# Kernel optimization log

Measured on AMD Instinct MI355X. Metric: run time of the kernel, lower is better.

Reference implementation:

```python
import jax, jax.numpy as jnp
import numpy as np

NS, NV, NB, L = 64, 32, 8, 4      # scalar channels, vector channels, bessel bases, layers
EMB = 32                           # atom-type embedding dim
MAX_R = 3.0                        # cutoff radius
NUM_NEIGH = 32.0                   # avg degree used for scatter normalization
N, E = 10000, 320000
NW = NS * 2 + NV * 2               # per-edge tensor-product weights from radial MLP
MAX_TYPES = 10


def smooth_cutoff(x):
    # e3nn md-example smooth_cutoff: 1 for x<0.5, 0 for x>1, cosine blend between
    u = 2.0 * (x - 1.0)
    y = (1.0 - jnp.cos(jnp.pi * u)) * 0.5
    y = jnp.where(u > 0.0, 0.0, y)
    y = jnp.where(u < -1.0, 1.0, y)
    return y


def bessel_basis(r):
    # soft_one_hot_linspace(basis='bessel', cutoff=False) * sqrt(NB)
    n = jnp.arange(1, NB + 1, dtype=r.dtype)
    y = jnp.sqrt(2.0 / MAX_R) * jnp.sin(n * jnp.pi * r[:, None] / MAX_R) / r[:, None]
    return y * np.sqrt(NB).astype(np.float32)


def edge_info(x, src, dst):
    feats, attrs = [], []
    for i in range(2):  # nvec = x.shape[-1] // 3 = 2
        vec = x[src, 3 * i:3 * i + 3] - x[dst, 3 * i:3 * i + 3]  # [E,3]
        r = jnp.linalg.norm(vec, axis=1)
        sh = np.float32(np.sqrt(3.0)) * vec / r[:, None]          # 1x1o SH, component norm
        feats.append(bessel_basis(r))
        attrs.append(smooth_cutoff(r / MAX_R)[:, None] * sh)
    return jnp.concatenate(feats, axis=-1), jnp.stack(attrs, axis=1)  # [E,2*NB], [E,2,3]


def _forward(x, emb_table, W_up, W_proj, fc1, b1, fc2, W_sv, W_vs, W_sc_s, W_sc_v, Ws, Wv, h, mix, node_attr, edge_src, edge_dst):
    n = x.shape[0]
    inv_nb = np.float32(1.0 / np.sqrt(NUM_NEIGH))
    # uplift: 2 input vectors -> NV hidden vectors, NS hidden scalars (zero init)
    xv = x.reshape(n, 2, 3)
    v = jnp.einsum('nic,iv->nvc', xv, W_up)        # [n,NV,3]
    s = jnp.zeros((n, NS), x.dtype)                # [n,NS]
    s_old, v_old = s, v
    attr_emb = emb_table[node_attr]                # [n,EMB]
    xcur = x
    for i in range(L):
        f, a = edge_info(xcur, edge_src, edge_dst)            # [E,2NB], [E,2,3]
        w = jax.nn.silu(f @ fc1[i] + b1[i]) @ fc2[i]          # [E,NW] radial TP weights
        w1 = w[:, :NS * 2].reshape(-1, NS, 2)                 # 0e x 1o -> 1o path weights
        w2 = w[:, NS * 2:].reshape(-1, NV, 2)                 # 1o x 1o -> 0e path weights
        # equivariant tensor-product messages (gather at edge_src)
        t = s[edge_src][:, :, None] * w1                      # [E,NS,2]
        q = jnp.einsum('euv,uvm->evm', t, W_sv[i])            # [E,2,NV]
        msg_v = jnp.einsum('evm,evc->emc', q, a)              # [E,NV,3]
        d = jnp.einsum('euc,evc->euv', v[edge_src], a)        # [E,NV,2]
        msg_s = jnp.einsum('euv,uvm->em', d * w2, W_vs[i])    # [E,NS+NV]
        # scatter-add at edge_dst, normalized by sqrt(num_neighbors)
        agg_s = jnp.zeros((n, NS + NV), x.dtype).at[edge_dst].add(msg_s) * inv_nb
        agg_v = jnp.zeros((n, NV, 3), x.dtype).at[edge_dst].add(msg_v) * inv_nb
        # self-connection: fully-connected TP with node-attr scalars
        sc_s = jnp.einsum('nu,ne,uem->nm', s, attr_emb, W_sc_s[i])
        sc_v = jnp.einsum('nuc,ne,uev->nvc', v, attr_emb, W_sc_v[i])
        cs = sc_s + agg_s
        cv = sc_v + agg_v
        # Gate: silu on scalars, sigmoid gate scalars modulate vectors
        gs = jax.nn.silu(cs[:, :NS])
        gate = jax.nn.sigmoid(cs[:, NS:])
        gv = cv * gate[:, :, None]
        # self-interaction (equivariant linear per degree)
        si_s = s @ Ws[i]
        si_v = jnp.einsum('nuc,uv->nvc', v, Wv[i])
        # verlet-like update
        hi2 = h[i] ** 2
        s_new = 2.0 * s - s_old + hi2 * (mix[i] * gs + (mix[i] - 1.0) * si_s)
        v_new = 2.0 * v - v_old + hi2 * (mix[i] * gv + (mix[i] - 1.0) * si_v)
        s_old, v_old = s, v
        s, v = s_new, v_new
        # project back to x for next layer's edge features
        xcur = jnp.einsum('nvc,vi->nic', v, W_proj).reshape(n, 6)
    return xcur


def setup_inputs() -> dict:
    key = jax.random.key(0)
    ks = jax.random.split(key, 20)
    x = jax.random.normal(ks[0], (N, 6), jnp.float32)
    node_attr = jax.random.randint(ks[1], (N,), 0, MAX_TYPES)
    edge_src = jax.random.randint(ks[2], (E,), 0, N)
    off = jax.random.randint(ks[3], (E,), 1, N)
    edge_dst = (edge_src + off) % N  # no self-loops -> no zero edge_vec
    batch = jnp.zeros((N,), jnp.int32)
    rn = lambda k, sh, sc: jax.random.normal(k, sh, jnp.float32) * np.float32(sc)
    emb_table = rn(ks[4], (MAX_TYPES, EMB), 0.5)
    W_up = rn(ks[5], (2, NV), 1.0 / np.sqrt(2))
    W_proj = rn(ks[6], (NV, 2), 1.0 / np.sqrt(NV))
    fc1 = rn(ks[7], (L, 2 * NB, 64), 1.0 / np.sqrt(2 * NB))
    b1 = jnp.zeros((L, 64), jnp.float32)
    fc2 = rn(ks[8], (L, 64, NW), 1.0 / np.sqrt(64))
    W_sv = rn(ks[9], (L, NS, 2, NV), 1.0 / np.sqrt(NS * 2))
    W_vs = rn(ks[10], (L, NV, 2, NS + NV), 1.0 / np.sqrt(NV * 2))
    W_sc_s = rn(ks[11], (L, NS, EMB, NS + NV), 1.0 / np.sqrt(NS * EMB))
    W_sc_v = rn(ks[12], (L, NV, EMB, NV), 1.0 / np.sqrt(NV * EMB))
    Ws = rn(ks[13], (L, NS, NS), 1.0 / np.sqrt(NS))
    Wv = rn(ks[14], (L, NV, NV), 1.0 / np.sqrt(NV))
    h = jnp.ones((L,), jnp.float32) * 0.01
    mix = jnp.ones((L,), jnp.float32) * 0.5
    return {"x": x, "emb_table": emb_table, "W_up": W_up, "W_proj": W_proj, "fc1": fc1, "b1": b1, "fc2": fc2, "W_sv": W_sv, "W_vs": W_vs, "W_sc_s": W_sc_s, "W_sc_v": W_sc_v, "Ws": Ws, "Wv": Wv, "h": h, "mix": mix, "node_attr": node_attr, "edge_src": edge_src, "edge_dst": edge_dst, "batch": batch}


def reference(x, emb_table, W_up, W_proj, fc1, b1, fc2, W_sv, W_vs, W_sc_s, W_sc_v, Ws, Wv, h, mix, node_attr, edge_src, edge_dst, batch):
    return _forward(x, emb_table, W_up, W_proj, fc1, b1, fc2, W_sv, W_vs, W_sc_s, W_sc_v, Ws, Wv, h, mix, node_attr, edge_src, edge_dst)
```

## Files before the change

### kernel.cpp

```cpp
#include <hip/hip_runtime.h>
#include <math.h>

constexpr int cNS = 64, cNV = 32, cNB = 8, cL = 4, cEMB = 32, cNT = 10;
constexpr float PI_F = 3.14159265358979323846f;
constexpr float INV_SQRT_NN = 0.17677669529663687f;
constexpr float BESSEL_C = 2.3094010767585034f;
constexpr float SQRT3 = 1.7320508075688772f;

typedef unsigned short u16;
typedef unsigned int u32;
typedef unsigned long long u64;
typedef __attribute__((ext_vector_type(8))) short bf16x8;
typedef __attribute__((ext_vector_type(4))) float f32x4;
typedef __attribute__((ext_vector_type(2))) float f32x2;
typedef __attribute__((ext_vector_type(4))) int i32x4;

__device__ __forceinline__ u16 f2b(float x) {
  u32 u = __float_as_uint(x);
  return (u16)((u + 0x7fffu + ((u >> 16) & 1u)) >> 16);
}
__device__ __forceinline__ float b2f(u16 h) { return __uint_as_float(((u32)h) << 16); }
__device__ __forceinline__ float blo(u32 w) { return __uint_as_float(w << 16); }
__device__ __forceinline__ float bhi(u32 w) { return __uint_as_float(w & 0xffff0000u); }

__device__ __forceinline__ u32 pkbf(float lo, float hi) {
  u32 r;
  asm("v_cvt_pk_bf16_f32 %0, %1, %2" : "=v"(r) : "v"(lo), "v"(hi));
  return r;
}

__device__ __forceinline__ void lds_fence() {
  asm volatile("s_waitcnt lgkmcnt(0)" ::: "memory");
  __builtin_amdgcn_sched_barrier(0);
}

union U8 { bf16x8 v; u32 w[4]; };

__device__ __forceinline__ f32x4 mfma16(bf16x8 a, bf16x8 b, f32x4 c) {
  return __builtin_amdgcn_mfma_f32_16x16x32_bf16(a, b, c, 0, 0, 0);
}


__global__ void k_precompA(const float* __restrict__ emb, const float* __restrict__ Wss,
                           float* __restrict__ A) {
  int idx = blockIdx.x * 256 + threadIdx.x;
  if (idx >= cL * cNT * 64 * 96) return;
  int m = idx % 96;
  int u = (idx / 96) % 64;
  int t = (idx / (96 * 64)) % cNT;
  int l = idx / (96 * 64 * cNT);
  float acc = 0.f;
#pragma unroll
  for (int e = 0; e < 32; ++e)
    acc += emb[t * 32 + e] * Wss[((size_t)(l * 64 + u) * 32 + e) * 96 + m];
  A[idx] = acc;
}

__global__ void k_precompB(const float* __restrict__ emb, const float* __restrict__ Wsv_,
                           float* __restrict__ B) {
  int idx = blockIdx.x * 256 + threadIdx.x;
  if (idx >= cL * cNT * 32 * 32) return;
  int vo = idx % 32;
  int u = (idx / 32) % 32;
  int t = (idx / 1024) % cNT;
  int l = idx / (1024 * cNT);
  float acc = 0.f;
#pragma unroll
  for (int e = 0; e < 32; ++e)
    acc += emb[t * 32 + e] * Wsv_[((size_t)(l * 32 + u) * 32 + e) * 32 + vo];
  B[idx] = acc;
}

__global__ void k_packB(const float* __restrict__ fc2, const float* __restrict__ Wsv,
                        const float* __restrict__ Wvs, const float* __restrict__ fc1,
                        u16* __restrict__ fc2L, u16* __restrict__ WsvL,
                        u16* __restrict__ WvsL, u16* __restrict__ fc1L) {
  int idx = blockIdx.x * 256 + threadIdx.x;
  const int T1 = cL * 12288, T2 = cL * 2 * 2048, T3 = cL * 2 * 3072, T4 = cL * 2048;
  if (idx < T1) {
    int l = idx / 12288, r = idx % 12288;
    int ki = r & 7, tt = r >> 3;
    int nn = tt % 192, kq = tt / 192;
    fc2L[idx] = f2b(fc2[((size_t)(l * 64) + kq * 8 + ki) * 192 + nn]);
  } else if (idx < T1 + T2) {
    int r0 = idx - T1;
    int l = r0 / 4096, r1 = r0 % 4096;
    int k2 = r1 / 2048, r = r1 % 2048;
    int ki = r & 7, tt = r >> 3;
    int mm = tt % 32, kq = tt / 32;
    WsvL[r0] = f2b(Wsv[((size_t)((l * 64 + kq * 8 + ki) * 2) + k2) * 32 + mm]);
  } else if (idx < T1 + T2 + T3) {
    int r0 = idx - T1 - T2;
    int l = r0 / 6144, r1 = r0 % 6144;
    int k2 = r1 / 3072, r = r1 % 3072;
    int ki = r & 7, tt = r >> 3;
    int mm = tt % 96, kq = tt / 96;
    WvsL[r0] = f2b(Wvs[((size_t)((l * 32 + kq * 8 + ki) * 2) + k2) * 96 + mm]);
  } else if (idx < T1 + T2 + T3 + T4) {
    int r0 = idx - T1 - T2 - T3;
    int l = r0 / 2048, r1 = r0 % 2048;
    int kq = r1 / 512, rem = r1 % 512;
    int n = rem / 8, ki = rem & 7;
    fc1L[r0] = (kq < 2) ? f2b(fc1[l * 1024 + (kq * 8 + ki) * 64 + n]) : (u16)0;
  }
}

__global__ void k_init(const float* __restrict__ x, const float* __restrict__ Wup,
                       float* __restrict__ v, float* __restrict__ v_old,
                       float* __restrict__ xcur, int N) {
  int idx = blockIdx.x * 256 + threadIdx.x;
  if (idx >= N * 32) return;
  int n = idx >> 5, vc = idx & 31;
  float w0 = Wup[vc], w1 = Wup[32 + vc];
#pragma unroll
  for (int c = 0; c < 3; ++c) {
    float val = x[n * 6 + c] * w0 + x[n * 6 + 3 + c] * w1;
    v[idx * 3 + c] = val;
    v_old[idx * 3 + c] = val;
  }
  if (vc < 6) xcur[n * 6 + vc] = x[n * 6 + vc];
}


__global__ void k_zero_i(int* __restrict__ p, int n) {
  int i = blockIdx.x * 256 + threadIdx.x;
  if (i < n) p[i] = 0;
}

__global__ void k_hist(const int* __restrict__ edst, int* __restrict__ deg, int E) {
  int e = blockIdx.x * 256 + threadIdx.x;
  if (e < E) atomicAdd(&deg[edst[e]], 1);
}

__global__ __launch_bounds__(1024) void k_scan(const int* __restrict__ deg,
                                               int* __restrict__ row_ptr,
                                               int* __restrict__ cursor, int N) {
  __shared__ int part[1024];
  int t = threadIdx.x;
  int chunk = (N + 1023) / 1024;
  int base = t * chunk;
  int sum = 0;
  for (int i = 0; i < chunk; ++i) {
    int idx = base + i;
    if (idx < N) sum += deg[idx];
  }
  part[t] = sum;
  __syncthreads();
  for (int off = 1; off < 1024; off <<= 1) {
    int val = (t >= off) ? part[t - off] : 0;
    __syncthreads();
    part[t] += val;
    __syncthreads();
  }
  int run = (t > 0) ? part[t - 1] : 0;
  for (int i = 0; i < chunk; ++i) {
    int idx = base + i;
    if (idx < N) {
      row_ptr[idx] = run;
      cursor[idx] = run;
      run += deg[idx];
    }
  }
  if (t == 1023) row_ptr[N] = part[1023];
}

__global__ void k_scatter(const int* __restrict__ esrc, const int* __restrict__ edst,
                          int* __restrict__ cursor, int* __restrict__ esrc_s,
                          int* __restrict__ edst_s, int E) {
  int e = blockIdx.x * 256 + threadIdx.x;
  if (e < E) {
    int d = edst[e];
    int p = atomicAdd(&cursor[d], 1);
    esrc_s[p] = esrc[e];
    edst_s[p] = d;
  }
}

template <bool SZERO>
__global__ __launch_bounds__(128) void k_edge_mfma(
    const float* __restrict__ xcur, const float* __restrict__ s, const float* __restrict__ v,
    const int* __restrict__ esrc_s, const int* __restrict__ edst_s,
    const u16* __restrict__ fc1L, const float* __restrict__ b1,
    const u16* __restrict__ fc2L, const u16* __restrict__ WsvL0,
    const u16* __restrict__ WsvL1, const u16* __restrict__ WvsL0,
    const u16* __restrict__ WvsL1, u16* __restrict__ msgbuf, int E) {
  __shared__ u16 wbAll[2][32 * 200];
  __shared__ float aAll[2][32][6];
  int wid = threadIdx.x >> 6, lane = threadIdx.x & 63;
  int e0 = (blockIdx.x * 2 + wid) * 32;
  if (e0 >= E) return;
  u16* wb = wbAll[wid];
  int lrow = lane & 15, lg = lane >> 4;

  {
    int el = lane >> 1, qq = lane & 1;
    int ge = e0 + el;
    if (ge >= E) ge = E - 1;
    int gs = esrc_s[ge], gd = edst_s[ge];
    const float* ps = xcur + (size_t)gs * 6 + qq * 3;
    const float* pd = xcur + (size_t)gd * 6 + qq * 3;
    float vx = ps[0] - pd[0];
    float vy = ps[1] - pd[1];
    float vz = ps[2] - pd[2];
    float r2 = vx * vx + vy * vy + vz * vz;
    float rr = sqrtf(r2);
    float invr = 1.0f / rr;
    float th = (PI_F / 3.0f) * rr;
    float s1, c1;
    __sincosf(th, &s1, &c1);
    float twc = 2.0f * c1;
    float snm = 0.f, sn = s1;
    float fc = BESSEL_C * invr;
    float f8[8];
#pragma unroll
    for (int nn = 0; nn < 8; ++nn) {
      f8[nn] = fc * sn;
      float nx = twc * sn - snm;
      snm = sn;
      sn = nx;
    }
    float uu = (2.0f / 3.0f) * rr - 2.0f;
    float cut;
    if (uu > 0.f) cut = 0.f;
    else if (uu < -1.f) cut = 1.f;
    else cut = (1.0f - __cosf(PI_F * uu)) * 0.5f;
    float sc = cut * SQRT3 * invr;
    u32* fp = (u32*)(wb + 5120 + el * 40);
#pragma unroll
    for (int i = 0; i < 4; ++i) fp[qq * 4 + i] = pkbf(f8[2 * i], f8[2 * i + 1]);
#pragma unroll
    for (int i = 0; i < 4; ++i) fp[8 + qq * 4 + i] = 0u;
    float* ap = aAll[wid][el];
    ap[qq * 3 + 0] = vx * sc;
    ap[qq * 3 + 1] = vy * sc;
    ap[qq * 3 + 2] = vz * sc;
  }
  lds_fence();

  {
    bf16x8 fA0 = *(const bf16x8*)(wb + 5120 + lrow * 40 + lg * 8);
    bf16x8 fA1 = *(const bf16x8*)(wb + 5120 + (16 + lrow) * 40 + lg * 8);
    f32x4 hp0[4], hp1[4];
#pragma unroll
    for (int nb = 0; nb < 4; ++nb) {
      bf16x8 bB = *(const bf16x8*)(fc1L + (size_t)(lg * 64 + nb * 16 + lrow) * 8);
      f32x4 z = {0.f, 0.f, 0.f, 0.f};
      hp0[nb] = mfma16(fA0, bB, z);
      hp1[nb] = mfma16(fA1, bB, z);
    }
#pragma unroll
    for (int nb = 0; nb < 4; ++nb) {
      float bias = b1[nb * 16 + lrow];
      int col = nb * 16 + lrow;
      {
        float hv[4];
#pragma unroll
        for (int r = 0; r < 4; ++r) {
          float xv = hp0[nb][r] + bias;
          hv[r] = xv * (1.0f / (1.0f + __expf(-xv)));
        }
        u32 p01 = pkbf(hv[0], hv[1]);
        u32 p23 = pkbf(hv[2], hv[3]);
        wb[(4 * lg + 0) * 72 + col] = (u16)p01;
        wb[(4 * lg + 1) * 72 + col] = (u16)(p01 >> 16);
        wb[(4 * lg + 2) * 72 + col] = (u16)p23;
        wb[(4 * lg + 3) * 72 + col] = (u16)(p23 >> 16);
      }
      {
        float hv[4];
#pragma unroll
        for (int r = 0; r < 4; ++r) {
          float xv = hp1[nb][r] + bias;
          hv[r] = xv * (1.0f / (1.0f + __expf(-xv)));
        }
        u32 p01 = pkbf(hv[0], hv[1]);
        u32 p23 = pkbf(hv[2], hv[3]);
        wb[(16 + 4 * lg + 0) * 72 + col] = (u16)p01;
        wb[(16 + 4 * lg + 1) * 72 + col] = (u16)(p01 >> 16);
        wb[(16 + 4 * lg + 2) * 72 + col] = (u16)p23;
        wb[(16 + 4 * lg + 3) * 72 + col] = (u16)(p23 >> 16);
      }
    }
  }
  lds_fence();

  bf16x8 ha0 = *(const bf16x8*)(wb + lrow * 72 + lg * 8);
  bf16x8 hbf0 = *(const bf16x8*)(wb + lrow * 72 + 32 + lg * 8);
  bf16x8 ha1 = *(const bf16x8*)(wb + (16 + lrow) * 72 + lg * 8);
  bf16x8 hbf1 = *(const bf16x8*)(wb + (16 + lrow) * 72 + 32 + lg * 8);
  lds_fence();

  int xw = lg << 3;
#pragma unroll
  for (int nb = (SZERO ? 8 : 0); nb < 12; ++nb) {
    bf16x8 b0 = *(const bf16x8*)(fc2L + (size_t)(lg * 192 + nb * 16 + lrow) * 8);
    bf16x8 b1v = *(const bf16x8*)(fc2L + (size_t)((4 + lg) * 192 + nb * 16 + lrow) * 8);
    f32x4 z = {0.f, 0.f, 0.f, 0.f};
    f32x4 c0 = mfma16(ha0, b0, z);
    c0 = mfma16(hbf0, b1v, c0);
    f32x4 c1 = mfma16(ha1, b0, z);
    c1 = mfma16(hbf1, b1v, c1);
    int n = nb * 16 + lrow;
    int pn = (n < 128) ? ((n & 1) * 64 + (n >> 1)) : (128 + (n & 1) * 32 + ((n - 128) >> 1));
    int cx = pn ^ xw;
    {
      int rb = (4 * lg) * 200 + cx;
      u32 p01 = pkbf(c0[0], c0[1]);
      u32 p23 = pkbf(c0[2], c0[3]);
      wb[rb] = (u16)p01;
      wb[rb + 200] = (u16)(p01 >> 16);
      wb[rb + 400] = (u16)p23;
      wb[rb + 600] = (u16)(p23 >> 16);
    }
    {
      int rb = (16 + 4 * lg) * 200 + cx;
      u32 p01 = pkbf(c1[0], c1[1]);
      u32 p23 = pkbf(c1[2], c1[3]);
      wb[rb] = (u16)p01;
      wb[rb + 200] = (u16)(p01 >> 16);
      wb[rb + 400] = (u16)p23;
      wb[rb + 600] = (u16)(p23 >> 16);
    }
  }
  lds_fence();

  const u16* wrow0 = wb + lrow * 200 + (((lg ^ (lrow >> 2)) & 3) << 3);
  const u16* wrow1 = wrow0 + 3200;

  int prow0 = e0 + lrow;
  if (prow0 >= E) prow0 = E - 1;
  int prow1 = e0 + 16 + lrow;
  if (prow1 >= E) prow1 = E - 1;
  int srcs[2] = {esrc_s[prow0], esrc_s[prow1]};

  f32x4 q0[2][2], q1[2][2];
  if (!SZERO) {
    U8 t0a[2], t0b[2], t1a[2], t1b[2];
#pragma unroll
    for (int h = 0; h < 2; ++h) {
      const u16* wr = h ? wrow1 : wrow0;
      const float* sp = s + (size_t)srcs[h] * 64;
      float sv0[8], sv1[8];
      *(f32x4*)(sv0) = *(const f32x4*)(sp + lg * 8);
      *(f32x4*)(sv0 + 4) = *(const f32x4*)(sp + lg * 8 + 4);
      *(f32x4*)(sv1) = *(const f32x4*)(sp + 32 + lg * 8);
      *(f32x4*)(sv1 + 4) = *(const f32x4*)(sp + 32 + lg * 8 + 4);
      i32x4 W0a = *(const i32x4*)(wr);
      i32x4 W0b = *(const i32x4*)(wr + 32);
      i32x4 W1a = *(const i32x4*)(wr + 64);
      i32x4 W1b = *(const i32x4*)(wr + 96);
#pragma unroll
      for (int j2 = 0; j2 < 4; ++j2) {
        u32 wa = (u32)W0a[j2], wbv = (u32)W0b[j2], wc = (u32)W1a[j2], wd = (u32)W1b[j2];
        t0a[h].w[j2] = pkbf(sv0[2 * j2] * blo(wa), sv0[2 * j2 + 1] * bhi(wa));
        t0b[h].w[j2] = pkbf(sv1[2 * j2] * blo(wbv), sv1[2 * j2 + 1] * bhi(wbv));
        t1a[h].w[j2] = pkbf(sv0[2 * j2] * blo(wc), sv0[2 * j2 + 1] * bhi(wc));
        t1b[h].w[j2] = pkbf(sv1[2 * j2] * blo(wd), sv1[2 * j2 + 1] * bhi(wd));
      }
    }
#pragma unroll
    for (int nb = 0; nb < 2; ++nb) {
      bf16x8 bA = *(const bf16x8*)(WsvL0 + (size_t)(lg * 32 + nb * 16 + lrow) * 8);
      bf16x8 bB = *(const bf16x8*)(WsvL0 + (size_t)((4 + lg) * 32 + nb * 16 + lrow) * 8);
      bf16x8 bC = *(const bf16x8*)(WsvL1 + (size_t)(lg * 32 + nb * 16 + lrow) * 8);
      bf16x8 bD = *(const bf16x8*)(WsvL1 + (size_t)((4 + lg) * 32 + nb * 16 + lrow) * 8);
#pragma unroll
      for (int h = 0; h < 2; ++h) {
        f32x4 z = {0.f, 0.f, 0.f, 0.f};
        f32x4 c = mfma16(t0a[h].v, bA, z);
        c = mfma16(t0b[h].v, bB, c);
        q0[h][nb] = c;
        f32x4 c2 = mfma16(t1a[h].v, bC, z);
        c2 = mfma16(t1b[h].v, bD, c2);
        q1[h][nb] = c2;
      }
    }
  }

  U8 ga[2], gb[2];
#pragma unroll
  for (int h = 0; h < 2; ++h) {
    const float* ap = aAll[wid][h * 16 + lrow];
    float a00 = ap[0], a01 = ap[1], a02 = ap[2], a10 = ap[3], a11 = ap[4], a12 = ap[5];
    float vl[24];
    const float* vp = v + (size_t)srcs[h] * 96 + lg * 24;
#pragma unroll
    for (int i = 0; i < 6; ++i) *(f32x4*)(vl + 4 * i) = *(const f32x4*)(vp + 4 * i);
    const u16* wr = h ? wrow1 : wrow0;
    i32x4 W2a = *(const i32x4*)(wr + 128);
    i32x4 W2b = *(const i32x4*)(wr + 160);
#pragma unroll
    for (int j2 = 0; j2 < 4; ++j2) {
      float d0a, d1a, d0b, d1b;
      {
        float vx = vl[6 * j2 + 0], vy = vl[6 * j2 + 1], vz = vl[6 * j2 + 2];
        d0a = vx * a00 + vy * a01 + vz * a02;
        d1a = vx * a10 + vy * a11 + vz * a12;
      }
      {
        float vx = vl[6 * j2 + 3], vy = vl[6 * j2 + 4], vz = vl[6 * j2 + 5];
        d0b = vx * a00 + vy * a01 + vz * a02;
        d1b = vx * a10 + vy * a11 + vz * a12;
      }
      u32 wa = (u32)W2a[j2], wbv = (u32)W2b[j2];
      ga[h].w[j2] = pkbf(d0a * blo(wa), d0b * bhi(wa));
      gb[h].w[j2] = pkbf(d1a * blo(wbv), d1b * bhi(wbv));
    }
  }
  f32x4 mS[2][6];
#pragma unroll
  for (int nb = 0; nb < 6; ++nb) {
    bf16x8 b0 = *(const bf16x8*)(WvsL0 + (size_t)(lg * 96 + nb * 16 + lrow) * 8);
    bf16x8 b1v = *(const bf16x8*)(WvsL1 + (size_t)(lg * 96 + nb * 16 + lrow) * 8);
#pragma unroll
    for (int h = 0; h < 2; ++h) {
      f32x4 z = {0.f, 0.f, 0.f, 0.f};
      f32x4 c = mfma16(ga[h].v, b0, z);
      c = mfma16(gb[h].v, b1v, c);
      mS[h][nb] = c;
    }
  }

  lds_fence();
#pragma unroll
  for (int h = 0; h < 2; ++h) {
    int rbase = (h * 16 + 4 * lg) * 200;
#pragma unroll
    for (int nb = 0; nb < 6; ++nb) {
      u32 p01 = pkbf(mS[h][nb][0], mS[h][nb][1]);
      u32 p23 = pkbf(mS[h][nb][2], mS[h][nb][3]);
      int colx = (nb * 16 + lrow) ^ xw;
      wb[rbase + colx] = (u16)p01;
      wb[rbase + 200 + colx] = (u16)(p01 >> 16);
      wb[rbase + 400 + colx] = (u16)p23;
      wb[rbase + 600 + colx] = (u16)(p23 >> 16);
    }
    if (!SZERO) {
#pragma unroll
      for (int nb = 0; nb < 2; ++nb) {
#pragma unroll
        for (int r = 0; r < 4; ++r) {
          int el = h * 16 + 4 * lg + r;
          const float* ap = aAll[wid][el];
          float Q0v = q0[h][nb][r], Q1v = q1[h][nb][r];
          float v0 = Q0v * ap[0] + Q1v * ap[3];
          float v1 = Q0v * ap[1] + Q1v * ap[4];
          float v2 = Q0v * ap[2] + Q1v * ap[5];
          u32 p01 = pkbf(v0, v1);
          int base = el * 200 + ((96 + nb * 16 + lrow) ^ xw);
          wb[base] = (u16)p01;
          wb[base + 32] = (u16)(p01 >> 16);
          wb[base + 64] = f2b(v2);
        }
      }
    }
  }
  lds_fence();

  int orow = lane >> 1, oq = lane & 1;
  if (e0 + orow < E) {
    const int OST = SZERO ? 96 : 192;
    u16* gdst = msgbuf + (size_t)(e0 + orow) * OST;
    int xo = ((orow >> 2) & 3) << 3;
    const int NIT = SZERO ? 6 : 12;
#pragma unroll
    for (int it = 0; it < NIT; ++it) {
      int col = oq * 8 + it * 16;
      i32x4 d = *(const i32x4*)(wb + orow * 200 + (col ^ xo));
      *(i32x4*)(gdst + col) = d;
    }
  }
}

template <bool SZERO>
__global__ __launch_bounds__(256) void k_gnode(
    const u16* __restrict__ msg, const int* __restrict__ row_ptr,
    float* __restrict__ s, float* __restrict__ sold, float* __restrict__ v,
    float* __restrict__ vold,
    const float* __restrict__ Amat, const float* __restrict__ Bmat,
    const float* __restrict__ Ws, const float* __restrict__ Wv,
    const float* __restrict__ Wproj, const int* __restrict__ nattr,
    const float* __restrict__ hArr, const float* __restrict__ mixArr, int layer,
    float* __restrict__ xout, int N) {
  int half = threadIdx.x >> 7;
  int t = threadIdx.x & 127;
  int n = blockIdx.x * 2 + half;
  bool active = n < N;
  if (!active) n = N - 1;
  __shared__ float agg[2][192];
  __shared__ float srow[2][64];
  __shared__ float vrow[2][96];
  __shared__ float gateS[2][32];
  __shared__ float vnewS[2][96];
  int start = row_ptr[n], end = row_ptr[n + 1];
  const int STRIDE = SZERO ? 96 : 192;
  int nacc4 = SZERO ? 24 : 48;
  if (t < nacc4) {
    const u16* mp = msg + (size_t)t * 4;
    float accA[4] = {0.f, 0.f, 0.f, 0.f};
    float accB[4] = {0.f, 0.f, 0.f, 0.f};
    int p = start;
    for (; p + 8 <= end; p += 8) {
      u64 w[8];
#pragma unroll
      for (int k = 0; k < 8; ++k) w[k] = *(const u64*)(mp + (size_t)(p + k) * STRIDE);
#pragma unroll
      for (int k = 0; k < 8; ++k) {
        u32 wl = (u32)w[k], wh = (u32)(w[k] >> 32);
        float* acc = (k & 1) ? accB : accA;
        acc[0] += blo(wl);
        acc[1] += bhi(wl);
        acc[2] += blo(wh);
        acc[3] += bhi(wh);
      }
    }
    for (; p < end; ++p) {
      u64 w = *(const u64*)(mp + (size_t)p * STRIDE);
      u32 wl = (u32)w, wh = (u32)(w >> 32);
      accA[0] += blo(wl);
      accA[1] += bhi(wl);
      accA[2] += blo(wh);
      accA[3] += bhi(wh);
    }
#pragma unroll
    for (int c = 0; c < 4; ++c)
      agg[half][4 * t + c] = (accA[c] + accB[c]) * INV_SQRT_NN;
  }
  if (SZERO && t >= 24 && t < 48) {
#pragma unroll
    for (int c = 0; c < 4; ++c) agg[half][4 * t + c] = 0.f;
  }
  if (t < 64) srow[half][t] = s[(size_t)n * 64 + t];
  if (t < 96) vrow[half][t] = v[(size_t)n * 96 + t];
  __syncthreads();
  int type = nattr[n];
  float hv = hArr[layer];
  float h2v = hv * hv;
  float mx = mixArr[layer];
  float cs = 0.f;
  if (t < 96) {
    cs = agg[half][t];
    const float* Ac = Amat + (size_t)type * 64 * 96 + t;
#pragma unroll 8
    for (int u = 0; u < 64; ++u) cs += srow[half][u] * Ac[u * 96];
  }
  if (t >= 64 && t < 96) gateS[half][t - 64] = 1.0f / (1.0f + __expf(-cs));
  __syncthreads();
  if (t < 64) {
    float gs = cs * (1.0f / (1.0f + __expf(-cs)));
    float sis = 0.f;
#pragma unroll 8
    for (int u = 0; u < 64; ++u) sis += srow[half][u] * Ws[u * 64 + t];
    float scur = srow[half][t];
    float sprev = sold[(size_t)n * 64 + t];
    float snew = 2.f * scur - sprev + h2v * (mx * gs + (mx - 1.f) * sis);
    if (active) {
      sold[(size_t)n * 64 + t] = scur;
      s[(size_t)n * 64 + t] = snew;
    }
  }
  if (t < 96) {
    int vch = t / 3, c = t - vch * 3;
    float cv = agg[half][96 + c * 32 + vch];
    const float* Bc = Bmat + (size_t)type * 1024 + vch;
    float scv = 0.f, siv = 0.f;
#pragma unroll 8
    for (int u = 0; u < 32; ++u) {
      float vu = vrow[half][u * 3 + c];
      scv += vu * Bc[u * 32];
      siv += vu * Wv[u * 32 + vch];
    }
    cv += scv;
    float gv = cv * gateS[half][vch];
    float vcur = vrow[half][t];
    float vprev = vold[(size_t)n * 96 + t];
    float vnew = 2.f * vcur - vprev + h2v * (mx * gv + (mx - 1.f) * siv);
    if (active) {
      vold[(size_t)n * 96 + t] = vcur;
      v[(size_t)n * 96 + t] = vnew;
    }
    vnewS[half][t] = vnew;
  }
  __syncthreads();
  if (t < 6 && active) {
    int i = t / 3, c = t - i * 3;
    float acc = 0.f;
#pragma unroll
    for (int vo = 0; vo < 32; ++vo) acc += vnewS[half][vo * 3 + c] * Wproj[vo * 2 + i];
    xout[(size_t)n * 6 + t] = acc;
  }
}

extern "C" void kernel_launch(void* const* d_in, const int* in_sizes, int n_in,
                              void* d_out, int out_size, void* d_ws, size_t ws_size,
                              hipStream_t stream) {
  const float* x = (const float*)d_in[0];
  const float* emb = (const float*)d_in[1];
  const float* Wup = (const float*)d_in[2];
  const float* Wproj = (const float*)d_in[3];
  const float* fc1 = (const float*)d_in[4];
  const float* b1 = (const float*)d_in[5];
  const float* fc2 = (const float*)d_in[6];
  const float* Wsv = (const float*)d_in[7];
  const float* Wvs = (const float*)d_in[8];
  const float* Wscs = (const float*)d_in[9];
  const float* Wscv = (const float*)d_in[10];
  const float* Ws = (const float*)d_in[11];
  const float* Wv = (const float*)d_in[12];
  const float* hArr = (const float*)d_in[13];
  const float* mixArr = (const float*)d_in[14];
  const int* nattr = (const int*)d_in[15];
  const int* esrc = (const int*)d_in[16];
  const int* edst = (const int*)d_in[17];

  const int N = in_sizes[0] / 6;
  const int E = in_sizes[16];

  float* ws = (float*)d_ws;
  size_t off = 0;
  auto alloc = [&](size_t nf) {
    float* p = ws + off;
    off += (nf + 3) & ~(size_t)3;
    return p;
  };
  float* sbuf = alloc((size_t)N * 64);
  float* sold = alloc((size_t)N * 64);
  float* vbuf = alloc((size_t)N * 96);
  float* vold = alloc((size_t)N * 96);
  float* xcur = alloc((size_t)N * 6);
  float* Amat = alloc((size_t)cL * cNT * 64 * 96);
  float* Bmat = alloc((size_t)cL * cNT * 32 * 32);
  u16* fc2L = (u16*)alloc((size_t)cL * 6144);
  u16* WsvL = (u16*)alloc((size_t)cL * 2048);
  u16* WvsL = (u16*)alloc((size_t)cL * 3072);
  u16* fc1L = (u16*)alloc((size_t)cL * 1024);
  int* deg = (int*)alloc((size_t)(N + 4));
  int* row_ptr = (int*)alloc((size_t)(N + 4));
  int* cursor = (int*)alloc((size_t)(N + 4));
  int* esrc_s = (int*)alloc((size_t)E);
  int* edst_s = (int*)alloc((size_t)E);
  u16* msgbuf = (u16*)alloc((size_t)E * 96);

  hipMemsetAsync(sbuf, 0, sizeof(float) * (size_t)N * 128, stream);
  k_init<<<(N * 32 + 255) / 256, 256, 0, stream>>>(x, Wup, vbuf, vold, xcur, N);
  k_precompA<<<(cL * cNT * 64 * 96 + 255) / 256, 256, 0, stream>>>(emb, Wscs, Amat);
  k_precompB<<<(cL * cNT * 32 * 32 + 255) / 256, 256, 0, stream>>>(emb, Wscv, Bmat);
  {
    int tot = cL * 12288 + cL * 4096 + cL * 6144 + cL * 2048;
    k_packB<<<(tot + 255) / 256, 256, 0, stream>>>(fc2, Wsv, Wvs, fc1, fc2L, WsvL, WvsL, fc1L);
  }
  k_zero_i<<<(N + 255) / 256, 256, 0, stream>>>(deg, N);
  k_hist<<<(E + 255) / 256, 256, 0, stream>>>(edst, deg, E);
  k_scan<<<1, 1024, 0, stream>>>(deg, row_ptr, cursor, N);
  k_scatter<<<(E + 255) / 256, 256, 0, stream>>>(esrc, edst, cursor, esrc_s, edst_s, E);

  int eblocks = (E + 63) / 64;
  int gblocks = (N + 1) / 2;
  for (int l = 0; l < cL; ++l) {
    if (l == 0)
      k_edge_mfma<true><<<eblocks, 128, 0, stream>>>(
          xcur, sbuf, vbuf, esrc_s, edst_s, fc1L + l * 2048, b1 + l * 64,
          fc2L + l * 12288, WsvL + l * 4096, WsvL + l * 4096 + 2048,
          WvsL + l * 6144, WvsL + l * 6144 + 3072, msgbuf, E);
    else
      k_edge_mfma<false><<<eblocks, 128, 0, stream>>>(
          xcur, sbuf, vbuf, esrc_s, edst_s, fc1L + l * 2048, b1 + l * 64,
          fc2L + l * 12288, WsvL + l * 4096, WsvL + l * 4096 + 2048,
          WvsL + l * 6144, WvsL + l * 6144 + 3072, msgbuf, E);
    float* xout = (l == cL - 1) ? (float*)d_out : xcur;
    if (l == 0)
      k_gnode<true><<<gblocks, 256, 0, stream>>>(
          msgbuf, row_ptr, sbuf, sold, vbuf, vold, Amat + (size_t)l * cNT * 64 * 96,
          Bmat + (size_t)l * cNT * 1024, Ws + l * 4096, Wv + l * 1024, Wproj, nattr,
          hArr, mixArr, l, xout, N);
    else
      k_gnode<false><<<gblocks, 256, 0, stream>>>(
          msgbuf, row_ptr, sbuf, sold, vbuf, vold, Amat + (size_t)l * cNT * 64 * 96,
          Bmat + (size_t)l * cNT * 1024, Ws + l * 4096, Wv + l * 1024, Wproj, nattr,
          hArr, mixArr, l, xout, N);
  }
}
```

Before: 556.9 us.

## Fuse per-edge message aggregation into edge kernel via segmented atomic adds

The edge kernel no longer writes a bf16 message per edge for the node kernel to gather through CSR. Edges are already sorted by destination, so each warp now sums its 32 messages in a running segmented reduction and flushes them with float atomicAdd into a per-node fp32 buffer. That buffer is zeroed each layer, and the node kernel just reads it. This removes the large per-edge message round trip through memory, at the cost of atomics, an extra memset per layer and non-deterministic summation order.

```diff
diff --git a/kernel.cpp b/kernel.cpp
--- a/kernel.cpp
+++ b/kernel.cpp
@@ -183,9 +183,10 @@
     const u16* __restrict__ fc1L, const float* __restrict__ b1,
     const u16* __restrict__ fc2L, const u16* __restrict__ WsvL0,
     const u16* __restrict__ WsvL1, const u16* __restrict__ WvsL0,
-    const u16* __restrict__ WvsL1, u16* __restrict__ msgbuf, int E) {
+    const u16* __restrict__ WvsL1, float* __restrict__ aggbuf, int E) {
   __shared__ u16 wbAll[2][32 * 200];
   __shared__ float aAll[2][32][6];
+  __shared__ int dAll[2][32];
   int wid = threadIdx.x >> 6, lane = threadIdx.x & 63;
   int e0 = (blockIdx.x * 2 + wid) * 32;
   if (e0 >= E) return;
@@ -234,6 +235,7 @@
     ap[qq * 3 + 0] = vx * sc;
     ap[qq * 3 + 1] = vy * sc;
     ap[qq * 3 + 2] = vz * sc;
+    if (qq == 0) dAll[wid][el] = gd;
   }
   lds_fence();
 
@@ -457,24 +459,40 @@
   }
   lds_fence();
 
-  int orow = lane >> 1, oq = lane & 1;
-  if (e0 + orow < E) {
-    const int OST = SZERO ? 96 : 192;
-    u16* gdst = msgbuf + (size_t)(e0 + orow) * OST;
-    int xo = ((orow >> 2) & 3) << 3;
-    const int NIT = SZERO ? 6 : 12;
-#pragma unroll
-    for (int it = 0; it < NIT; ++it) {
-      int col = oq * 8 + it * 16;
-      i32x4 d = *(const i32x4*)(wb + orow * 200 + (col ^ xo));
-      *(i32x4*)(gdst + col) = d;
-    }
-  }
-}
-
-template <bool SZERO>
+  {
+    int nrows = E - e0;
+    if (nrows > 32) nrows = 32;
+    const int* dstv = dAll[wid];
+    int c0 = lane, c1 = lane + 64, c2 = lane + 128;
+    bool v1ok = SZERO ? (c1 < 96) : true;
+    bool v2ok = SZERO ? false : true;
+    float acc0 = 0.f, acc1 = 0.f, acc2 = 0.f;
+    int prev = dstv[0];
+    for (int r = 0; r < nrows; ++r) {
+      int d = dstv[r];
+      if (d != prev) {
+        float* ab = aggbuf + (size_t)prev * 192;
+        atomicAdd(ab + c0, acc0);
+        if (v1ok) atomicAdd(ab + c1, acc1);
+        if (v2ok) atomicAdd(ab + c2, acc2);
+        acc0 = acc1 = acc2 = 0.f;
+        prev = d;
+      }
+      int xo = ((r >> 2) & 3) << 3;
+      int rb = r * 200;
+      acc0 += b2f(wb[rb + (c0 ^ xo)]);
+      if (v1ok) acc1 += b2f(wb[rb + (c1 ^ xo)]);
+      if (v2ok) acc2 += b2f(wb[rb + (c2 ^ xo)]);
+    }
+    float* ab = aggbuf + (size_t)prev * 192;
+    atomicAdd(ab + c0, acc0);
+    if (v1ok) atomicAdd(ab + c1, acc1);
+    if (v2ok) atomicAdd(ab + c2, acc2);
+  }
+}
+
 __global__ __launch_bounds__(256) void k_gnode(
-    const u16* __restrict__ msg, const int* __restrict__ row_ptr,
+    const float* __restrict__ aggbuf,
     float* __restrict__ s, float* __restrict__ sold, float* __restrict__ v,
     float* __restrict__ vold,
     const float* __restrict__ Amat, const float* __restrict__ Bmat,
@@ -492,43 +510,9 @@
   __shared__ float vrow[2][96];
   __shared__ float gateS[2][32];
   __shared__ float vnewS[2][96];
-  int start = row_ptr[n], end = row_ptr[n + 1];
-  const int STRIDE = SZERO ? 96 : 192;
-  int nacc4 = SZERO ? 24 : 48;
-  if (t < nacc4) {
-    const u16* mp = msg + (size_t)t * 4;
-    float accA[4] = {0.f, 0.f, 0.f, 0.f};
-    float accB[4] = {0.f, 0.f, 0.f, 0.f};
-    int p = start;
-    for (; p + 8 <= end; p += 8) {
-      u64 w[8];
-#pragma unroll
-      for (int k = 0; k < 8; ++k) w[k] = *(const u64*)(mp + (size_t)(p + k) * STRIDE);
-#pragma unroll
-      for (int k = 0; k < 8; ++k) {
-        u32 wl = (u32)w[k], wh = (u32)(w[k] >> 32);
-        float* acc = (k & 1) ? accB : accA;
-        acc[0] += blo(wl);
-        acc[1] += bhi(wl);
-        acc[2] += blo(wh);
-        acc[3] += bhi(wh);
-      }
-    }
-    for (; p < end; ++p) {
-      u64 w = *(const u64*)(mp + (size_t)p * STRIDE);
-      u32 wl = (u32)w, wh = (u32)(w >> 32);
-      accA[0] += blo(wl);
-      accA[1] += bhi(wl);
-      accA[2] += blo(wh);
-      accA[3] += bhi(wh);
-    }
-#pragma unroll
-    for (int c = 0; c < 4; ++c)
-      agg[half][4 * t + c] = (accA[c] + accB[c]) * INV_SQRT_NN;
-  }
-  if (SZERO && t >= 24 && t < 48) {
-#pragma unroll
-    for (int c = 0; c < 4; ++c) agg[half][4 * t + c] = 0.f;
+  if (t < 96) {
+    agg[half][t] = aggbuf[(size_t)n * 192 + t] * INV_SQRT_NN;
+    agg[half][96 + t] = aggbuf[(size_t)n * 192 + 96 + t] * INV_SQRT_NN;
   }
   if (t < 64) srow[half][t] = s[(size_t)n * 64 + t];
   if (t < 96) vrow[half][t] = v[(size_t)n * 96 + t];
@@ -628,6 +612,7 @@
   float* vbuf = alloc((size_t)N * 96);
   float* vold = alloc((size_t)N * 96);
   float* xcur = alloc((size_t)N * 6);
+  float* aggbuf = alloc((size_t)N * 192);
   float* Amat = alloc((size_t)cL * cNT * 64 * 96);
   float* Bmat = alloc((size_t)cL * cNT * 32 * 32);
   u16* fc2L = (u16*)alloc((size_t)cL * 6144);
@@ -639,7 +624,6 @@
   int* cursor = (int*)alloc((size_t)(N + 4));
   int* esrc_s = (int*)alloc((size_t)E);
   int* edst_s = (int*)alloc((size_t)E);
-  u16* msgbuf = (u16*)alloc((size_t)E * 96);
 
   hipMemsetAsync(sbuf, 0, sizeof(float) * (size_t)N * 128, stream);
   k_init<<<(N * 32 + 255) / 256, 256, 0, stream>>>(x, Wup, vbuf, vold, xcur, N);
@@ -657,26 +641,21 @@
   int eblocks = (E + 63) / 64;
   int gblocks = (N + 1) / 2;
   for (int l = 0; l < cL; ++l) {
+    hipMemsetAsync(aggbuf, 0, sizeof(float) * (size_t)N * 192, stream);
     if (l == 0)
       k_edge_mfma<true><<<eblocks, 128, 0, stream>>>(
           xcur, sbuf, vbuf, esrc_s, edst_s, fc1L + l * 2048, b1 + l * 64,
           fc2L + l * 12288, WsvL + l * 4096, WsvL + l * 4096 + 2048,
-          WvsL + l * 6144, WvsL + l * 6144 + 3072, msgbuf, E);
+          WvsL + l * 6144, WvsL + l * 6144 + 3072, aggbuf, E);
     else
       k_edge_mfma<false><<<eblocks, 128, 0, stream>>>(
           xcur, sbuf, vbuf, esrc_s, edst_s, fc1L + l * 2048, b1 + l * 64,
           fc2L + l * 12288, WsvL + l * 4096, WsvL + l * 4096 + 2048,
-          WvsL + l * 6144, WvsL + l * 6144 + 3072, msgbuf, E);
+          WvsL + l * 6144, WvsL + l * 6144 + 3072, aggbuf, E);
     float* xout = (l == cL - 1) ? (float*)d_out : xcur;
-    if (l == 0)
-      k_gnode<true><<<gblocks, 256, 0, stream>>>(
-          msgbuf, row_ptr, sbuf, sold, vbuf, vold, Amat + (size_t)l * cNT * 64 * 96,
-          Bmat + (size_t)l * cNT * 1024, Ws + l * 4096, Wv + l * 1024, Wproj, nattr,
-          hArr, mixArr, l, xout, N);
-    else
-      k_gnode<false><<<gblocks, 256, 0, stream>>>(
-          msgbuf, row_ptr, sbuf, sold, vbuf, vold, Amat + (size_t)l * cNT * 64 * 96,
-          Bmat + (size_t)l * cNT * 1024, Ws + l * 4096, Wv + l * 1024, Wproj, nattr,
-          hArr, mixArr, l, xout, N);
-  }
-}
+    k_gnode<<<gblocks, 256, 0, stream>>>(
+        aggbuf, sbuf, sold, vbuf, vold, Amat + (size_t)l * cNT * 64 * 96,
+        Bmat + (size_t)l * cNT * 1024, Ws + l * 4096, Wv + l * 1024, Wproj, nattr,
+        hArr, mixArr, l, xout, N);
+  }
+}
```

Result: faster. 517.7 us (-7.0%).
